# Kernel optimization log

Hardware: AMD Instinct MI355X
Metric: run time of the kernel (lower is better)

The kernel has to match this reference:

```python
import jax, jax.numpy as jnp
import numpy as np
from math import pi

# Static config derived from init_kwargs and x's shape
N = 1024                 # support (frame length)
STRIDE = 256
B = 64
L = 160000
T = 1 + (L - (N - 1) - 1) // STRIDE   # 622 frames
POW = 1.0                # spectrum magnitude power
WIN_MIN = N / 20.0
WIN_MAX = float(N)
STRIDE_MIN = 0.0
STRIDE_MAX = float(N)


def setup_inputs() -> dict:
    key = jax.random.key(0)
    kx, = jax.random.split(key, 1)
    x = jax.random.normal(kx, (B, L), dtype=jnp.float32)
    win_length = jnp.full((1,), 1024.0, dtype=jnp.float32)
    strides = jnp.full((1,), 256.0, dtype=jnp.float32)
    win_pow = jnp.full((1,), 1.0, dtype=jnp.float32)
    return {"x": x, "win_length": win_length, "strides": strides, "win_pow": win_pow}


def reference(x, win_length, strides, win_pow):
    dtype = x.dtype
    # --- parameter transforms (clamp) ---
    wl = jnp.clip(win_length, WIN_MIN, WIN_MAX)          # (1,)
    st = jnp.clip(strides, STRIDE_MIN, STRIDE_MAX)       # (1,)

    # --- frame start positions: frames[0]=0, frames[t]=cumsum of strides ---
    es = jnp.broadcast_to(st, (T,))
    frames = jnp.concatenate([jnp.zeros((1,), dtype=es.dtype), jnp.cumsum(es[1:])])  # (T,)

    idx_floor_f = jnp.floor(frames)
    idx_frac = frames - idx_floor_f                       # (T,) fractional shift

    # --- gather overlapping frames with out-of-range zeroing ---
    idx = idx_floor_f.astype(jnp.int32)[:, None] + jnp.arange(N, dtype=jnp.int32)  # (T, N)
    valid = (idx < L) & (idx >= 0)
    gathered = jnp.take(x, jnp.clip(idx, 0, L - 1), axis=1)  # (B, T, N)
    strided_x = jnp.where(valid[None, :, :], gathered, jnp.zeros((), dtype))

    # --- fractional-shift Hann window, per frame ---
    base = jnp.arange(N, dtype=dtype)[:, None] - idx_frac[None, :]  # (N, T)
    tap = 0.5 - 0.5 * jnp.cos(2.0 * pi * (base + (wl - N + 1) / 2.0) / wl)
    mask1 = base >= jnp.ceil((N - 1 + wl) / 2.0)
    mask2 = base <= jnp.floor((N - 1 - wl) / 2.0)
    tap = jnp.where(mask1 | mask2, jnp.zeros((), dtype), tap)
    tap = tap / jnp.sum(tap, axis=0, keepdims=True)       # normalize per frame
    tap = tap ** win_pow                                   # (N, T)
    tap_win = tap.T[None, :, :]                            # (1, T, N)

    # --- taper, rFFT, magnitude^pow ---
    tapered = strided_x * tap_win                          # (B, T, N)
    spec = jnp.abs(jnp.fft.rfft(tapered, axis=-1)) ** POW  # (B, T, F)
    return jnp.transpose(spec, (0, 2, 1))                  # (B, F, T)
```

## Files before the change

### kernel.cpp

```cpp
#include <hip/hip_runtime.h>
#include <math.h>

#define NN 1024
#define B_C 64
#define L_C 160000
#define T_C 622
#define F_C 513
#define TT 16
#define NTILE ((T_C + TT - 1) / TT)
#define WIN_MIN_C (1024.0f / 20.0f)
#define WIN_MAX_C 1024.0f
#define TWO_PI 6.28318530717958647692f

typedef unsigned uv2 __attribute__((ext_vector_type(2)));
typedef float v2f __attribute__((ext_vector_type(2)));

__device__ __forceinline__ int brev6(int x) {
    return ((x & 1) << 5) | ((x & 2) << 3) | ((x & 4) << 1) |
           ((x & 8) >> 1) | ((x & 16) >> 3) | ((x & 32) >> 5);
}

__device__ __forceinline__ v2f cmul_pk(v2f d, v2f cs) {
    v2f t, r;
    asm("v_pk_mul_f32 %0, %1, %2 op_sel_hi:[1,0]"
        : "=v"(t) : "v"(d), "v"(cs));
    asm("v_pk_fma_f32 %0, %1, %2, %3 op_sel:[1,1,0] op_sel_hi:[0,1,1] neg_lo:[1,0,0]"
        : "=v"(r) : "v"(d), "v"(cs), "v"(t));
    return r;
}

__device__ __forceinline__ float lane_xor32(float v, int l) {
#if __has_builtin(__builtin_amdgcn_permlane32_swap)
    uv2 r = __builtin_amdgcn_permlane32_swap(__float_as_uint(v), __float_as_uint(v),
                                             false, false);
    return __uint_as_float((l & 32) ? r.x : r.y);
#else
    return __shfl_xor(v, 32, 64);
#endif
}
__device__ __forceinline__ float lane_xor16(float v, int l) {
#if __has_builtin(__builtin_amdgcn_permlane16_swap)
    uv2 r = __builtin_amdgcn_permlane16_swap(__float_as_uint(v), __float_as_uint(v),
                                             false, false);
    return __uint_as_float((l & 16) ? r.x : r.y);
#else
    return __shfl_xor(v, 16, 64);
#endif
}
__device__ __forceinline__ float lane_xor8(float v) {
    return __int_as_float(__builtin_amdgcn_update_dpp(
        __float_as_int(v), __float_as_int(v), 0x128, 0xF, 0xF, false));
}
__device__ __forceinline__ float lane_xor4(float v) {
    return __int_as_float(__builtin_amdgcn_ds_swizzle(__float_as_int(v), 0x101F));
}
__device__ __forceinline__ float lane_xor2(float v) {
    return __int_as_float(__builtin_amdgcn_update_dpp(
        __float_as_int(v), __float_as_int(v), 0x4E, 0xF, 0xF, false));
}
__device__ __forceinline__ float lane_xor1(float v) {
    return __int_as_float(__builtin_amdgcn_update_dpp(
        __float_as_int(v), __float_as_int(v), 0xB1, 0xF, 0xF, false));
}
__device__ __forceinline__ float lane_mirror16(float v) {
    return __int_as_float(__builtin_amdgcn_update_dpp(
        __float_as_int(v), __float_as_int(v), 0x140, 0xF, 0xF, false));
}
__device__ __forceinline__ float lane_xor63(float v, int l) {
    return lane_xor32(lane_xor16(lane_mirror16(v), l), l);
}
__device__ __forceinline__ float fast_sqrtf(float x) {
#if __has_builtin(__builtin_amdgcn_sqrtf)
    return __builtin_amdgcn_sqrtf(x);
#else
    return sqrtf(x);
#endif
}

__global__ __launch_bounds__(256) void win_kernel(
    const float* __restrict__ win_length,
    const float* __restrict__ strides,
    const float* __restrict__ win_pow,
    float* __restrict__ tap)
{
    const int t = blockIdx.x;
    const int tid = threadIdx.x;

    const float wl = fminf(fmaxf(win_length[0], WIN_MIN_C), WIN_MAX_C);
    const float st = fminf(fmaxf(strides[0], 0.0f), WIN_MAX_C);
    const float wp = win_pow[0];

    const float frame = (float)t * st;
    const float frac = frame - floorf(frame);

    const float hi = ceilf(((float)NN - 1.0f + wl) * 0.5f);
    const float lo = floorf(((float)NN - 1.0f - wl) * 0.5f);
    const float off = (wl - (float)NN + 1.0f) * 0.5f;
    const float inv_wl = 1.0f / wl;

    __shared__ float s_tap[NN];
    __shared__ float s_red[256];

    float local = 0.0f;
    for (int n = tid; n < NN; n += 256) {
        float base = (float)n - frac;
        float v = 0.5f - 0.5f * cosf(TWO_PI * (base + off) * inv_wl);
        if (base >= hi || base <= lo) v = 0.0f;
        s_tap[n] = v;
        local += v;
    }
    s_red[tid] = local;
    __syncthreads();
    for (int s = 128; s > 0; s >>= 1) {
        if (tid < s) s_red[tid] += s_red[tid + s];
        __syncthreads();
    }
    const float inv_sum = 1.0f / s_red[0];
    const bool pow_one = (wp == 1.0f);
    for (int n = tid; n < NN; n += 256) {
        float v = s_tap[n] * inv_sum;
        if (!pow_one) v = powf(v, wp);
        tap[t * NN + n] = 0.5f * v;
    }
}

__global__ __launch_bounds__(512, 4) void fftw_kernel(
    const float* __restrict__ x,
    const float* __restrict__ strides,
    const float* __restrict__ tap,
    float* __restrict__ out)
{
    const int tile = blockIdx.x % NTILE;
    const int b = blockIdx.x / NTILE;
    const int t0 = tile * TT;
    const int tid = threadIdx.x;
    const int w = tid >> 6;
    const int l = tid & 63;

    const float st = fminf(fmaxf(strides[0], 0.0f), WIN_MAX_C);
    const float* xb = x + (size_t)b * L_C;

    __shared__ float mag[TT][F_C + 16];

    const int bl = brev6(l);
    const int l2 = brev6((64 - bl) & 63);

    constexpr int BR4[16]     = {0,8,4,12,2,10,6,14,1,9,5,13,3,11,7,15};
    constexpr int PARTNER[16] = {0,1,3,2,7,6,5,4,15,14,13,12,11,10,9,8};
    constexpr float C16[8] = {1.0f, 0.92387953251f, 0.70710678119f, 0.38268343236f,
                              0.0f, -0.38268343236f, -0.70710678119f, -0.92387953251f};
    constexpr float S16[8] = {0.0f, -0.38268343236f, -0.70710678119f, -0.92387953251f,
                              -1.0f, -0.92387953251f, -0.70710678119f, -0.38268343236f};

    const int jp = w;
    const int tA = t0 + 2 * jp;
    const int tB = tA + 1;
    const bool hasA = (tA < T_C);
    const bool hasB = (tB < T_C);
    const int idxA = hasA ? (int)floorf((float)tA * st) : 0;
    const int idxB = hasB ? (int)floorf((float)tB * st) : 0;
    const float* tpA = tap + (size_t)tA * NN;
    const float* tpB = tap + (size_t)tB * NN;

    v2f v[16];

    const bool okA = hasA && (idxA >= 0) && (idxA + NN <= L_C);
    const bool okB = hasB && (idxB >= 0) && (idxB + NN <= L_C);
    if (okA && okB) {
#pragma unroll
        for (int r = 0; r < 16; ++r) {
            const int n = r * 64 + l;
            v[r].x = xb[idxA + n] * tpA[n];
            v[r].y = xb[idxB + n] * tpB[n];
        }
    } else {
#pragma unroll
        for (int r = 0; r < 16; ++r) {
            const int n = r * 64 + l;
            float a = 0.0f, bb = 0.0f;
            if (hasA) {
                int ia = idxA + n;
                a = (ia >= 0 && ia < L_C) ? xb[ia] * tpA[n] : 0.0f;
            }
            if (hasB) {
                int ib = idxB + n;
                bb = (ib >= 0 && ib < L_C) ? xb[ib] * tpB[n] : 0.0f;
            }
            v[r].x = a;
            v[r].y = bb;
        }
    }

#pragma unroll
    for (int s = 0; s < 4; ++s) {
        const int half = (16 >> s) >> 1;
#pragma unroll
        for (int b0 = 0; b0 < 16; b0 += (16 >> s)) {
#pragma unroll
            for (int j = 0; j < 8; ++j) {
                if (j < half) {
                    const int i0 = b0 + j, i1 = b0 + j + half;
                    const v2f u = v[i0], ww = v[i1];
                    v[i0] = u + ww;
                    const v2f d = u - ww;
                    if ((j << s) == 0) {
                        v[i1] = d;
                    } else {
                        v2f cs;
                        cs.x = C16[j << s];
                        cs.y = S16[j << s];
                        v[i1] = cmul_pk(d, cs);
                    }
                }
            }
        }
    }

    {
        float c1, s1;
        __sincosf(-(TWO_PI / 1024.0f) * (float)l, &s1, &c1);
        const float c2 = c1 * c1 - s1 * s1,  s2 = 2.0f * c1 * s1;
        const float c4 = c2 * c2 - s2 * s2,  s4 = 2.0f * c2 * s2;
        const float c8 = c4 * c4 - s4 * s4,  s8 = 2.0f * c4 * s4;
        const float c3 = c1 * c2 - s1 * s2,  s3 = c1 * s2 + s1 * c2;
        const float c5 = c1 * c4 - s1 * s4,  s5 = c1 * s4 + s1 * c4;
        const float c6 = c2 * c4 - s2 * s4,  s6 = c2 * s4 + s2 * c4;
        const float c7 = c3 * c4 - s3 * s4,  s7 = c3 * s4 + s3 * c4;
        const float c9  = c1 * c8 - s1 * s8, s9  = c1 * s8 + s1 * c8;
        const float c10 = c2 * c8 - s2 * s8, s10 = c2 * s8 + s2 * c8;
        const float c11 = c3 * c8 - s3 * s8, s11 = c3 * s8 + s3 * c8;
        const float c12 = c4 * c8 - s4 * s8, s12 = c4 * s8 + s4 * c8;
        const float c13 = c5 * c8 - s5 * s8, s13 = c5 * s8 + s5 * c8;
        const float c14 = c6 * c8 - s6 * s8, s14 = c6 * s8 + s6 * c8;
        const float c15 = c7 * c8 - s7 * s8, s15 = c7 * s8 + s7 * c8;
#define TW(K) { v2f cs; cs.x = c##K; cs.y = s##K; \
                v[BR4[K]] = cmul_pk(v[BR4[K]], cs); }
        TW(1) TW(2) TW(3) TW(4) TW(5) TW(6) TW(7) TW(8)
        TW(9) TW(10) TW(11) TW(12) TW(13) TW(14) TW(15)
#undef TW
    }

    {
        float cu, su;
        __sincosf(-(TWO_PI / 64.0f) * (float)l, &su, &cu);

        {
            const bool hi_ = (l & 32) != 0;
            const float sgn = hi_ ? -1.0f : 1.0f;
            v2f tcs; tcs.x = hi_ ? cu : 1.0f; tcs.y = hi_ ? su : 0.0f;
#pragma unroll
            for (int i = 0; i < 16; ++i) {
                v2f d;
#if __has_builtin(__builtin_amdgcn_permlane32_swap)
                uv2 xr = __builtin_amdgcn_permlane32_swap(
                    __float_as_uint(v[i].x), __float_as_uint(v[i].x), false, false);
                uv2 xi = __builtin_amdgcn_permlane32_swap(
                    __float_as_uint(v[i].y), __float_as_uint(v[i].y), false, false);
                d.x = fmaf(sgn, __uint_as_float(xr.x), __uint_as_float(xr.y));
                d.y = fmaf(sgn, __uint_as_float(xi.x), __uint_as_float(xi.y));
#else
                d.x = fmaf(sgn, __shfl_xor(v[i].x, 32, 64), v[i].x);
                d.y = fmaf(sgn, __shfl_xor(v[i].y, 32, 64), v[i].y);
#endif
                v[i] = cmul_pk(d, tcs);
            }
            const float nc = fmaf(2.0f * cu, cu, -1.0f);
            su = 2.0f * cu * su; cu = nc;
        }
        {
            const bool hi_ = (l & 16) != 0;
            const float sgn = hi_ ? -1.0f : 1.0f;
            v2f tcs; tcs.x = hi_ ? cu : 1.0f; tcs.y = hi_ ? su : 0.0f;
#pragma unroll
            for (int i = 0; i < 16; ++i) {
                v2f d;
#if __has_builtin(__builtin_amdgcn_permlane16_swap)
                uv2 xr = __builtin_amdgcn_permlane16_swap(
                    __float_as_uint(v[i].x), __float_as_uint(v[i].x), false, false);
                uv2 xi = __builtin_amdgcn_permlane16_swap(
                    __float_as_uint(v[i].y), __float_as_uint(v[i].y), false, false);
                d.x = fmaf(sgn, __uint_as_float(xr.x), __uint_as_float(xr.y));
                d.y = fmaf(sgn, __uint_as_float(xi.x), __uint_as_float(xi.y));
#else
                d.x = fmaf(sgn, __shfl_xor(v[i].x, 16, 64), v[i].x);
                d.y = fmaf(sgn, __shfl_xor(v[i].y, 16, 64), v[i].y);
#endif
                v[i] = cmul_pk(d, tcs);
            }
            const float nc = fmaf(2.0f * cu, cu, -1.0f);
            su = 2.0f * cu * su; cu = nc;
        }
#define FOLD_STAGE(MASK, EXCH)                                                \
        {                                                                     \
            const bool hi_ = (l & (MASK)) != 0;                               \
            const float sgn = hi_ ? -1.0f : 1.0f;                             \
            v2f tcs; tcs.x = hi_ ? cu : 1.0f; tcs.y = hi_ ? su : 0.0f;        \
            _Pragma("unroll")                                                 \
            for (int i = 0; i < 16; ++i) {                                    \
                v2f d;                                                        \
                d.x = fmaf(sgn, EXCH(v[i].x), v[i].x);                        \
                d.y = fmaf(sgn, EXCH(v[i].y), v[i].y);                        \
                v[i] = cmul_pk(d, tcs);                                       \
            }                                                                 \
            const float nc = fmaf(2.0f * cu, cu, -1.0f);                      \
            su = 2.0f * cu * su; cu = nc;                                     \
        }
        FOLD_STAGE(8, lane_xor8)
        FOLD_STAGE(4, lane_xor4)
        FOLD_STAGE(2, lane_xor2)
#undef FOLD_STAGE
        {
            const float sgn = (l & 1) ? -1.0f : 1.0f;
#pragma unroll
            for (int i = 0; i < 16; ++i) {
                v[i].x = fmaf(sgn, v[i].x, lane_xor1(v[i].x));
                v[i].y = fmaf(sgn, v[i].y, lane_xor1(v[i].y));
            }
        }
    }

    {
        {
            const float yr = __shfl(v[0].x, l2, 64);
            const float yi = __shfl(v[0].y, l2, 64);
            const int k = 16 * bl;
            if (k <= 512) {
                const float sa = v[0].x + yr, sb = v[0].y - yi;
                const float ua = v[0].y + yi, ub = yr - v[0].x;
                const int ka = k + (k >> 5);
                if (hasA) mag[2 * jp][ka] = fast_sqrtf(fmaf(sa, sa, sb * sb));
                if (hasB) mag[2 * jp + 1][ka] = fast_sqrtf(fmaf(ua, ua, ub * ub));
            }
        }
        const bool lowk = (bl < 32);
        v2f sp; sp.x = lowk ? 1.0f : -1.0f; sp.y = lowk ? -1.0f : 1.0f;
        const int row = 2 * jp + (lowk ? 0 : 1);
        const bool wr_ok = lowk ? hasA : hasB;
#pragma unroll
        for (int i = 1; i < 16; ++i) {
            v2f y;
            y.x = lane_xor63(v[PARTNER[i]].x, l);
            y.y = lane_xor63(v[PARTNER[i]].y, l);
            const v2f t = y * sp + v[i];
            const float m = fast_sqrtf(fmaf(t.x, t.x, t.y * t.y));
            const int kp = BR4[i] + 16 * bl;
            const int k = lowk ? kp : (NN - kp);
            const int ka = k + (k >> 5);
            if (wr_ok) mag[row][ka] = m;
        }
    }

    __syncthreads();

    if (t0 + TT <= T_C) {
        for (int q = tid; q < F_C * 8; q += 512) {
            const int f = q >> 3;
            const int tg = (q & 7) << 1;
            const int fa = f + (f >> 5);
            float2 o;
            o.x = mag[tg + 0][fa];
            o.y = mag[tg + 1][fa];
            *(float2*)&out[((size_t)b * F_C + f) * T_C + t0 + tg] = o;
        }
    } else {
        for (int e = tid; e < F_C * TT; e += 512) {
            const int f = e >> 4;
            const int tt = e & 15;
            const int t = t0 + tt;
            if (t < T_C)
                out[((size_t)b * F_C + f) * T_C + t] = mag[tt][f + (f >> 5)];
        }
    }
}

extern "C" void kernel_launch(void* const* d_in, const int* in_sizes, int n_in,
                              void* d_out, int out_size, void* d_ws, size_t ws_size,
                              hipStream_t stream) {
    const float* x   = (const float*)d_in[0];
    const float* wl  = (const float*)d_in[1];
    const float* st  = (const float*)d_in[2];
    const float* wp  = (const float*)d_in[3];
    float* out = (float*)d_out;
    float* tap = (float*)d_ws;

    win_kernel<<<dim3(T_C), dim3(256), 0, stream>>>(wl, st, wp, tap);
    fftw_kernel<<<dim3(B_C * NTILE), dim3(512), 0, stream>>>(x, st, tap, out);
}
```

Baseline: 73.56 us.

## Fuse Hann window generation into FFT kernel and drop separate window pass

```diff
diff --git a/kernel.cpp b/kernel.cpp
--- a/kernel.cpp
+++ b/kernel.cpp
@@ -62,12 +62,11 @@
     return __int_as_float(__builtin_amdgcn_update_dpp(
         __float_as_int(v), __float_as_int(v), 0xB1, 0xF, 0xF, false));
 }
-__device__ __forceinline__ float lane_mirror16(float v) {
-    return __int_as_float(__builtin_amdgcn_update_dpp(
-        __float_as_int(v), __float_as_int(v), 0x140, 0xF, 0xF, false));
+__device__ __forceinline__ float lane_xor31(float v) {
+    return __int_as_float(__builtin_amdgcn_ds_swizzle(__float_as_int(v), 0x7C1F));
 }
 __device__ __forceinline__ float lane_xor63(float v, int l) {
-    return lane_xor32(lane_xor16(lane_mirror16(v), l), l);
+    return lane_xor32(lane_xor31(v), l);
 }
 __device__ __forceinline__ float fast_sqrtf(float x) {
 #if __has_builtin(__builtin_amdgcn_sqrtf)
@@ -77,57 +76,11 @@
 #endif
 }
 
-__global__ __launch_bounds__(256) void win_kernel(
+__global__ __launch_bounds__(512, 4) void fftw_kernel(
+    const float* __restrict__ x,
     const float* __restrict__ win_length,
     const float* __restrict__ strides,
     const float* __restrict__ win_pow,
-    float* __restrict__ tap)
-{
-    const int t = blockIdx.x;
-    const int tid = threadIdx.x;
-
-    const float wl = fminf(fmaxf(win_length[0], WIN_MIN_C), WIN_MAX_C);
-    const float st = fminf(fmaxf(strides[0], 0.0f), WIN_MAX_C);
-    const float wp = win_pow[0];
-
-    const float frame = (float)t * st;
-    const float frac = frame - floorf(frame);
-
-    const float hi = ceilf(((float)NN - 1.0f + wl) * 0.5f);
-    const float lo = floorf(((float)NN - 1.0f - wl) * 0.5f);
-    const float off = (wl - (float)NN + 1.0f) * 0.5f;
-    const float inv_wl = 1.0f / wl;
-
-    __shared__ float s_tap[NN];
-    __shared__ float s_red[256];
-
-    float local = 0.0f;
-    for (int n = tid; n < NN; n += 256) {
-        float base = (float)n - frac;
-        float v = 0.5f - 0.5f * cosf(TWO_PI * (base + off) * inv_wl);
-        if (base >= hi || base <= lo) v = 0.0f;
-        s_tap[n] = v;
-        local += v;
-    }
-    s_red[tid] = local;
-    __syncthreads();
-    for (int s = 128; s > 0; s >>= 1) {
-        if (tid < s) s_red[tid] += s_red[tid + s];
-        __syncthreads();
-    }
-    const float inv_sum = 1.0f / s_red[0];
-    const bool pow_one = (wp == 1.0f);
-    for (int n = tid; n < NN; n += 256) {
-        float v = s_tap[n] * inv_sum;
-        if (!pow_one) v = powf(v, wp);
-        tap[t * NN + n] = 0.5f * v;
-    }
-}
-
-__global__ __launch_bounds__(512, 4) void fftw_kernel(
-    const float* __restrict__ x,
-    const float* __restrict__ strides,
-    const float* __restrict__ tap,
     float* __restrict__ out)
 {
     const int tile = blockIdx.x % NTILE;
@@ -137,7 +90,16 @@
     const int w = tid >> 6;
     const int l = tid & 63;
 
+    const float wl = fminf(fmaxf(win_length[0], WIN_MIN_C), WIN_MAX_C);
     const float st = fminf(fmaxf(strides[0], 0.0f), WIN_MAX_C);
+    const float wp = win_pow[0];
+    const bool pow_one = (wp == 1.0f);
+
+    const float hib = ceilf(((float)NN - 1.0f + wl) * 0.5f);
+    const float lob = floorf(((float)NN - 1.0f - wl) * 0.5f);
+    const float off = (wl - (float)NN + 1.0f) * 0.5f;
+    const float inv_wl = 1.0f / wl;
+
     const float* xb = x + (size_t)b * L_C;
 
     __shared__ float mag[TT][F_C + 16];
@@ -157,34 +119,81 @@
     const int tB = tA + 1;
     const bool hasA = (tA < T_C);
     const bool hasB = (tB < T_C);
-    const int idxA = hasA ? (int)floorf((float)tA * st) : 0;
-    const int idxB = hasB ? (int)floorf((float)tB * st) : 0;
-    const float* tpA = tap + (size_t)tA * NN;
-    const float* tpB = tap + (size_t)tB * NN;
+    const float frameA = (float)tA * st;
+    const float fracA = frameA - floorf(frameA);
+    const float frameB = (float)tB * st;
+    const float fracB = frameB - floorf(frameB);
+    const int idxA = hasA ? (int)floorf(frameA) : 0;
+    const int idxB = hasB ? (int)floorf(frameB) : 0;
 
     v2f v[16];
 
     const bool okA = hasA && (idxA >= 0) && (idxA + NN <= L_C);
     const bool okB = hasB && (idxB >= 0) && (idxB + NN <= L_C);
-    if (okA && okB) {
+    if (okA && okB && pow_one) {
+        float sA = 0.0f, sB = 0.0f;
 #pragma unroll
         for (int r = 0; r < 16; ++r) {
             const int n = r * 64 + l;
-            v[r].x = xb[idxA + n] * tpA[n];
-            v[r].y = xb[idxB + n] * tpB[n];
-        }
+            const float baseA = (float)n - fracA;
+            float hA = 0.5f - 0.5f * __cosf(TWO_PI * (baseA + off) * inv_wl);
+            hA = (baseA >= hib || baseA <= lob) ? 0.0f : hA;
+            sA += hA;
+            v[r].x = xb[idxA + n] * hA;
+            const float baseB = (float)n - fracB;
+            float hB = 0.5f - 0.5f * __cosf(TWO_PI * (baseB + off) * inv_wl);
+            hB = (baseB >= hib || baseB <= lob) ? 0.0f : hB;
+            sB += hB;
+            v[r].y = xb[idxB + n] * hB;
+        }
+#pragma unroll
+        for (int m = 1; m < 64; m <<= 1) {
+            sA += __shfl_xor(sA, m, 64);
+            sB += __shfl_xor(sB, m, 64);
+        }
+        v2f sc; sc.x = 0.5f / sA; sc.y = 0.5f / sB;
+#pragma unroll
+        for (int r = 0; r < 16; ++r) v[r] = v[r] * sc;
     } else {
+        float sA = 0.0f, sB = 0.0f;
+#pragma unroll
+        for (int r = 0; r < 16; ++r) {
+            const int n = r * 64 + l;
+            const float baseA = (float)n - fracA;
+            float hA = 0.5f - 0.5f * __cosf(TWO_PI * (baseA + off) * inv_wl);
+            hA = (baseA >= hib || baseA <= lob) ? 0.0f : hA;
+            sA += hA;
+            const float baseB = (float)n - fracB;
+            float hB = 0.5f - 0.5f * __cosf(TWO_PI * (baseB + off) * inv_wl);
+            hB = (baseB >= hib || baseB <= lob) ? 0.0f : hB;
+            sB += hB;
+        }
+        for (int m = 1; m < 64; m <<= 1) {
+            sA += __shfl_xor(sA, m, 64);
+            sB += __shfl_xor(sB, m, 64);
+        }
+        const float iA = 1.0f / sA, iB = 1.0f / sB;
 #pragma unroll
         for (int r = 0; r < 16; ++r) {
             const int n = r * 64 + l;
             float a = 0.0f, bb = 0.0f;
             if (hasA) {
-                int ia = idxA + n;
-                a = (ia >= 0 && ia < L_C) ? xb[ia] * tpA[n] : 0.0f;
+                const float baseA = (float)n - fracA;
+                float hA = 0.5f - 0.5f * __cosf(TWO_PI * (baseA + off) * inv_wl);
+                hA = (baseA >= hib || baseA <= lob) ? 0.0f : hA;
+                float tpv = hA * iA;
+                if (!pow_one) tpv = powf(tpv, wp);
+                const int ia = idxA + n;
+                a = (ia >= 0 && ia < L_C) ? xb[ia] * (0.5f * tpv) : 0.0f;
             }
             if (hasB) {
-                int ib = idxB + n;
-                bb = (ib >= 0 && ib < L_C) ? xb[ib] * tpB[n] : 0.0f;
+                const float baseB = (float)n - fracB;
+                float hB = 0.5f - 0.5f * __cosf(TWO_PI * (baseB + off) * inv_wl);
+                hB = (baseB >= hib || baseB <= lob) ? 0.0f : hB;
+                float tpv = hB * iB;
+                if (!pow_one) tpv = powf(tpv, wp);
+                const int ib = idxB + n;
+                bb = (ib >= 0 && ib < L_C) ? xb[ib] * (0.5f * tpv) : 0.0f;
             }
             v[r].x = a;
             v[r].y = bb;
@@ -381,8 +390,6 @@
     const float* st  = (const float*)d_in[2];
     const float* wp  = (const float*)d_in[3];
     float* out = (float*)d_out;
-    float* tap = (float*)d_ws;
-
-    win_kernel<<<dim3(T_C), dim3(256), 0, stream>>>(wl, st, wp, tap);
-    fftw_kernel<<<dim3(B_C * NTILE), dim3(512), 0, stream>>>(x, st, tap, out);
-}
+
+    fftw_kernel<<<dim3(B_C * NTILE), dim3(512), 0, stream>>>(x, wl, st, wp, out);
+}
```

After: 67.01 us. -8.9%, faster.
